# Kernel tuning notes

Measured on AMD Instinct MI355X. Metric: run time of the kernel, lower is better.

## Reference

```python
import jax, jax.numpy as jnp
import numpy as np

COMMITMENT_WEIGHT = 1.0


def setup_inputs() -> dict:
    key = jax.random.key(0)
    k1, k2 = jax.random.split(key)
    clap_embeddings = jax.random.normal(k1, (16, 2048, 512), dtype=jnp.float32)
    # Learned codebooks for the 8 residual quantizer stages: [Q, C, D]
    codebooks = jax.random.normal(k2, (8, 1024, 512), dtype=jnp.float32)
    return {"clap_embeddings": clap_embeddings, "codebooks": codebooks}


def reference(clap_embeddings, codebooks):
    """Residual VQ: cascade of nearest-codebook lookups on the residual.
    Returns (quantized [B,T,D], indices [B,T,Q], commit_loss scalar)."""
    B, T, D = clap_embeddings.shape
    flat = clap_embeddings.reshape(-1, D)  # [N, D], N = B*T

    def step(carry, cb):
        residual, quant_acc = carry          # [N,D], [N,D]; cb: [C,D]
        cb_sq = jnp.sum(cb * cb, axis=-1)    # [C]
        # squared-dist argmin: ||r||^2 term is constant per row, drop it
        dists = cb_sq[None, :] - 2.0 * (residual @ cb.T)  # [N, C]
        idx = jnp.argmin(dists, axis=-1)     # [N]
        qv = cb[idx]                         # [N, D] gather
        # commitment loss: mse(detach(quantize), residual_input)
        loss = jnp.mean(jnp.square(jax.lax.stop_gradient(qv) - residual))
        # straight-through estimator
        qv_st = residual + jax.lax.stop_gradient(qv - residual)
        new_residual = residual - jax.lax.stop_gradient(qv)
        return (new_residual, quant_acc + qv_st), (idx, loss)

    init = (flat, jnp.zeros_like(flat))
    (_, quant_flat), (idx_q, losses) = jax.lax.scan(step, init, codebooks)

    quantized = quant_flat.reshape(B, T, D)
    indices = jnp.transpose(idx_q, (1, 0)).reshape(B, T, -1)  # [B, T, Q]
    commit_loss = jnp.sum(losses) * COMMITMENT_WEIGHT
    return quantized, indices, commit_loss
```

## Files before the change

### kernel.cpp

```cpp
#include <hip/hip_runtime.h>
#include <hip/hip_bf16.h>

#define NQ 8
#define NC 1024
#define ND 512
#define NROWTOT 32768
#define QOFF 16777216ULL
#define TAU2 0.05f
#define RST 260

typedef short short8 __attribute__((ext_vector_type(8)));
typedef float f32x16 __attribute__((ext_vector_type(16)));

__device__ __forceinline__ unsigned f2bf_u(float f) {
  unsigned u = __float_as_uint(f);
  return (u + 0x7FFFu + ((u >> 16) & 1u)) >> 16;
}
__device__ __forceinline__ void merge_in(float &d1, int &i1, float &d2, int &i2,
                                         float nd, int ni) {
  bool b1 = (nd < d1) || (nd == d1 && ni < i1);
  bool b2 = (nd < d2) || (nd == d2 && ni < i2);
  if (b1) { d2 = d1; i2 = i1; d1 = nd; i1 = ni; }
  else if (b2) { d2 = nd; i2 = ni; }
}

__global__ __launch_bounds__(256) void cbsq_kernel(const float* __restrict__ cbg,
                                                   float* __restrict__ ws) {
  const int tid = threadIdx.x, wv = tid >> 6, lane = tid & 63;
  const int cbase = blockIdx.x * 32 + wv * 8;
  for (int j = 0; j < 8; ++j) {
    const int c = cbase + j;
    const float4* p = reinterpret_cast<const float4*>(cbg + (size_t)c * ND + lane * 8);
    float4 a = p[0], b = p[1];
    float s = a.x*a.x + a.y*a.y + a.z*a.z + a.w*a.w
            + b.x*b.x + b.y*b.y + b.z*b.z + b.w*b.w;
    #pragma unroll
    for (int m = 1; m < 64; m <<= 1) s += __shfl_xor(s, m, 64);
    if (lane == 0) ws[c] = s;
  }
}

__global__ __launch_bounds__(256) void fmt_kernel(const float* __restrict__ cbg,
                                                  unsigned short* __restrict__ Bh,
                                                  unsigned short* __restrict__ Bl) {
  int t = blockIdx.x * 256 + threadIdx.x;
  int i16 = t & 1023, ks = (t >> 10) & 31, cp = (t >> 15) & 1, q = (t >> 16) & 7;
  int grp = i16 >> 9, col = i16 & 511, c = cp * 512 + col;
  const float* src = cbg + ((size_t)q * NC + c) * ND + ks * 16 + grp * 8;
  float4 a = reinterpret_cast<const float4*>(src)[0];
  float4 b = reinterpret_cast<const float4*>(src)[1];
  float v[8] = {a.x, a.y, a.z, a.w, b.x, b.y, b.z, b.w};
  unsigned short hv[8], lv[8];
  #pragma unroll
  for (int j = 0; j < 8; ++j) {
    unsigned hb = f2bf_u(v[j]);
    float hf = __uint_as_float(hb << 16);
    unsigned lb = f2bf_u(v[j] - hf);
    hv[j] = (unsigned short)hb; lv[j] = (unsigned short)lb;
  }
  size_t dst = (size_t)(t >> 10) * 8192 + (size_t)i16 * 8;
  uint4 wh, wl;
  wh.x = hv[0] | ((unsigned)hv[1] << 16); wh.y = hv[2] | ((unsigned)hv[3] << 16);
  wh.z = hv[4] | ((unsigned)hv[5] << 16); wh.w = hv[6] | ((unsigned)hv[7] << 16);
  wl.x = lv[0] | ((unsigned)lv[1] << 16); wl.y = lv[2] | ((unsigned)lv[3] << 16);
  wl.z = lv[4] | ((unsigned)lv[5] << 16); wl.w = lv[6] | ((unsigned)lv[7] << 16);
  *reinterpret_cast<uint4*>(Bh + dst) = wh;
  *reinterpret_cast<uint4*>(Bl + dst) = wl;
}

__global__ __launch_bounds__(256) void copy_kernel(const float4* __restrict__ src,
                                                   float4* __restrict__ dst) {
  int i = blockIdx.x * 256 + threadIdx.x;
  dst[i] = src[i];
}

__global__ __launch_bounds__(1024) __attribute__((amdgpu_waves_per_eu(4, 4)))
void dist_kernel(const float* __restrict__ resf, const float* __restrict__ cbsq_g,
                 const unsigned short* __restrict__ Bh,
                 const unsigned short* __restrict__ Bl,
                 float* __restrict__ t2d, int* __restrict__ t2i, int q) {
  __shared__ unsigned resH[64 * RST];
  __shared__ unsigned resL[64 * RST];
  __shared__ float mrgd[2][8][64][2];
  __shared__ int   mrgi[2][8][64][2];
  const int tid = threadIdx.x;
  const int w = tid >> 6, l = tid & 63;
  const int n0 = blockIdx.x * 64;
  const int rowbase = (w >> 3) * 32;
  const int colq = (w & 7) * 64;
  union U8 { uint4 q4; short8 s; unsigned u[4]; };

  {
    const float4* src = reinterpret_cast<const float4*>(resf) + (size_t)n0 * 128;
    #pragma unroll
    for (int j = 0; j < 8; ++j) {
      const int idx = j * 1024 + tid;
      float4 v = src[idx];
      const int row = idx >> 7, c4 = idx & 127;
      unsigned h0 = f2bf_u(v.x), g0 = f2bf_u(v.x - __uint_as_float(h0 << 16));
      unsigned h1 = f2bf_u(v.y), g1 = f2bf_u(v.y - __uint_as_float(h1 << 16));
      unsigned h2 = f2bf_u(v.z), g2 = f2bf_u(v.z - __uint_as_float(h2 << 16));
      unsigned h3 = f2bf_u(v.w), g3 = f2bf_u(v.w - __uint_as_float(h3 << 16));
      const int off = row * RST + c4 * 2;
      resH[off]     = h0 | (h1 << 16);
      resH[off + 1] = h2 | (h3 << 16);
      resL[off]     = g0 | (g1 << 16);
      resL[off + 1] = g2 | (g3 << 16);
    }
  }

  int baddr[2];
  #pragma unroll
  for (int t = 0; t < 2; ++t) {
    int i16 = ((l >> 5) << 9) + colq + t * 32 + (l & 31);
    baddr[t] = i16 * 8;
  }
  const int aoff0 = (rowbase + (l & 31)) * RST + ((l >> 5) << 2);
  __syncthreads();

  #pragma unroll 1
  for (int cp = 0; cp < 2; ++cp) {
    f32x16 acc[2];
    #pragma unroll
    for (int t = 0; t < 2; ++t)
      #pragma unroll
      for (int e = 0; e < 16; ++e) acc[t][e] = 0.f;

    const unsigned short* bhc = Bh + (size_t)((q * 2 + cp) * 32) * 8192;
    const unsigned short* blc = Bl + (size_t)((q * 2 + cp) * 32) * 8192;
    float sqv[2];
    #pragma unroll
    for (int t = 0; t < 2; ++t)
      sqv[t] = cbsq_g[q * NC + cp * 512 + colq + t * 32 + (l & 31)];

    uint4 fA[4], fB[4];

#define LOADB(buf, kk) { \
    const unsigned short* _h = bhc + (size_t)(kk) * 8192; \
    const unsigned short* _l = blc + (size_t)(kk) * 8192; \
    buf[0] = *reinterpret_cast<const uint4*>(_h + baddr[0]); \
    buf[1] = *reinterpret_cast<const uint4*>(_h + baddr[1]); \
    buf[2] = *reinterpret_cast<const uint4*>(_l + baddr[0]); \
    buf[3] = *reinterpret_cast<const uint4*>(_l + baddr[1]); }

#define DOSTEP(kk, buf) { \
    U8 Ah, Al; \
    const int _a = aoff0 + (kk) * 8; \
    Ah.q4 = *reinterpret_cast<const uint4*>(&resH[_a]); \
    Al.q4 = *reinterpret_cast<const uint4*>(&resL[_a]); \
    U8 b0h, b1h, b0l, b1l; \
    b0h.q4 = buf[0]; b1h.q4 = buf[1]; b0l.q4 = buf[2]; b1l.q4 = buf[3]; \
    acc[0] = __builtin_amdgcn_mfma_f32_32x32x16_bf16(Ah.s, b0h.s, acc[0], 0, 0, 0); \
    acc[0] = __builtin_amdgcn_mfma_f32_32x32x16_bf16(Al.s, b0h.s, acc[0], 0, 0, 0); \
    acc[0] = __builtin_amdgcn_mfma_f32_32x32x16_bf16(Ah.s, b0l.s, acc[0], 0, 0, 0); \
    acc[1] = __builtin_amdgcn_mfma_f32_32x32x16_bf16(Ah.s, b1h.s, acc[1], 0, 0, 0); \
    acc[1] = __builtin_amdgcn_mfma_f32_32x32x16_bf16(Al.s, b1h.s, acc[1], 0, 0, 0); \
    acc[1] = __builtin_amdgcn_mfma_f32_32x32x16_bf16(Ah.s, b1l.s, acc[1], 0, 0, 0); }

    LOADB(fA, 0);
    #pragma unroll 1
    for (int ks = 0; ks < 32; ks += 2) {
      LOADB(fB, ks + 1);
      DOSTEP(ks, fA);
      LOADB(fA, ks + 2 < 32 ? ks + 2 : 0);
      DOSTEP(ks + 1, fB);
    }
#undef LOADB
#undef DOSTEP

    #pragma unroll
    for (int rg2 = 0; rg2 < 16; ++rg2) {
      float d1 = INFINITY, d2 = INFINITY; int i1 = 0x7fffffff, i2 = 0x7fffffff;
      #pragma unroll
      for (int t = 0; t < 2; ++t) {
        int col = cp * 512 + colq + t * 32 + (l & 31);
        float dd = sqv[t] - 2.0f * acc[t][rg2];
        merge_in(d1, i1, d2, i2, dd, col);
      }
      #pragma unroll
      for (int m = 1; m < 32; m <<= 1) {
        float od1 = __shfl_xor(d1, m, 64), od2 = __shfl_xor(d2, m, 64);
        int oi1 = __shfl_xor(i1, m, 64), oi2 = __shfl_xor(i2, m, 64);
        merge_in(d1, i1, d2, i2, od1, oi1);
        merge_in(d1, i1, d2, i2, od2, oi2);
      }
      if ((l & 31) == 0) {
        int h = l >> 5;
        int rr = rowbase + (rg2 & 3) + 8 * (rg2 >> 2) + 4 * h;
        mrgd[cp][w & 7][rr][0] = d1; mrgd[cp][w & 7][rr][1] = d2;
        mrgi[cp][w & 7][rr][0] = i1; mrgi[cp][w & 7][rr][1] = i2;
      }
    }
  }
  __syncthreads();

  if (tid < 64) {
    float d1 = INFINITY, d2 = INFINITY; int i1 = 0x7fffffff, i2 = 0x7fffffff;
    #pragma unroll
    for (int c2 = 0; c2 < 2; ++c2)
      #pragma unroll
      for (int s2 = 0; s2 < 8; ++s2) {
        merge_in(d1, i1, d2, i2, mrgd[c2][s2][tid][0], mrgi[c2][s2][tid][0]);
        merge_in(d1, i1, d2, i2, mrgd[c2][s2][tid][1], mrgi[c2][s2][tid][1]);
      }
    t2d[(size_t)(n0 + tid) * 2 + 0] = d1;
    t2d[(size_t)(n0 + tid) * 2 + 1] = d2;
    t2i[(size_t)(n0 + tid) * 2 + 0] = i1;
    t2i[(size_t)(n0 + tid) * 2 + 1] = i2;
  }
}

__global__ __launch_bounds__(256) void upd_kernel(
    float* __restrict__ outf, const float* __restrict__ emb,
    const float* __restrict__ cbg, const float* __restrict__ t2d,
    const int* __restrict__ t2i, float* __restrict__ lpart, int q) {
  __shared__ int   fi_sh[64];
  __shared__ int   tlist[64][3];
  __shared__ int   tcount;
  __shared__ float red[256];
  const int tid = threadIdx.x;
  const int w = tid >> 6, l = tid & 63;
  const int n0 = blockIdx.x * 64;

  if (tid == 0) tcount = 0;
  __syncthreads();

  if (tid < 64) {
    float d1 = t2d[(size_t)(n0 + tid) * 2 + 0];
    float d2 = t2d[(size_t)(n0 + tid) * 2 + 1];
    int i1 = t2i[(size_t)(n0 + tid) * 2 + 0];
    int i2 = t2i[(size_t)(n0 + tid) * 2 + 1];
    int fi = i1 < 0 ? 0 : (i1 > NC - 1 ? NC - 1 : i1);
    int ib = i2 < 0 ? 0 : (i2 > NC - 1 ? NC - 1 : i2);
    fi_sh[tid] = fi;
    if (d2 - d1 < TAU2 && ib != fi) {
      int p = atomicAdd(&tcount, 1);
      tlist[p][0] = tid; tlist[p][1] = fi; tlist[p][2] = ib;
    }
  }
  __syncthreads();

  {
    int nt_ = tcount;
    for (int it = w; it < nt_; it += 4) {
      int rr = tlist[it][0], ia = tlist[it][1], ib = tlist[it][2];
      const float4* rp = reinterpret_cast<const float4*>(outf + (size_t)(n0 + rr) * ND + l * 8);
      float4 r0 = rp[0], r1 = rp[1];
      float rv[8] = {r0.x, r0.y, r0.z, r0.w, r1.x, r1.y, r1.z, r1.w};
      double da = 0.0, db = 0.0;
      {
        const float4* cr = reinterpret_cast<const float4*>(
            cbg + ((size_t)q * NC + ia) * ND + l * 8);
        float4 c0 = cr[0], c1 = cr[1];
        float cv[8] = {c0.x,c0.y,c0.z,c0.w,c1.x,c1.y,c1.z,c1.w};
        #pragma unroll
        for (int j = 0; j < 8; ++j) { double e = (double)cv[j] - (double)rv[j]; da += e * e; }
      }
      {
        const float4* cr = reinterpret_cast<const float4*>(
            cbg + ((size_t)q * NC + ib) * ND + l * 8);
        float4 c0 = cr[0], c1 = cr[1];
        float cv[8] = {c0.x,c0.y,c0.z,c0.w,c1.x,c1.y,c1.z,c1.w};
        #pragma unroll
        for (int j = 0; j < 8; ++j) { double e = (double)cv[j] - (double)rv[j]; db += e * e; }
      }
      #pragma unroll
      for (int m = 1; m < 64; m <<= 1) { da += __shfl_xor(da, m, 64); db += __shfl_xor(db, m, 64); }
      if (l == 0 && (db < da || (db == da && ib < ia))) fi_sh[rr] = ib;
    }
  }
  __syncthreads();

  if (tid < 64)
    outf[QOFF + (size_t)(n0 + tid) * NQ + q] = (float)fi_sh[tid];

  {
    const int row = tid >> 2, sg = tid & 3;
    const size_t base = (size_t)(n0 + row) * ND + sg * 128;
    float4* op = reinterpret_cast<float4*>(outf + base);
    const float4* cp4 = reinterpret_cast<const float4*>(
        cbg + ((size_t)q * NC + fi_sh[row]) * ND + sg * 128);
    const float4* ep = reinterpret_cast<const float4*>(emb + base);
    float ls = 0.f;
    #pragma unroll 4
    for (int i = 0; i < 32; ++i) {
      float4 r = op[i], c = cp4[i];
      float4 nr;
      nr.x = r.x - c.x; nr.y = r.y - c.y; nr.z = r.z - c.z; nr.w = r.w - c.w;
      ls += nr.x*nr.x + nr.y*nr.y + nr.z*nr.z + nr.w*nr.w;
      if (q < NQ - 1) {
        op[i] = nr;
      } else {
        float4 e = ep[i];
        float4 qv;
        qv.x = e.x - nr.x; qv.y = e.y - nr.y; qv.z = e.z - nr.z; qv.w = e.w - nr.w;
        op[i] = qv;
      }
    }
    red[tid] = ls;
  }
  __syncthreads();
  for (int s = 128; s > 0; s >>= 1) {
    if (tid < s) red[tid] += red[tid + s];
    __syncthreads();
  }
  if (tid == 0) lpart[blockIdx.x * NQ + q] = red[0];
}

__global__ __launch_bounds__(256) void loss_kernel(const float* __restrict__ lossws,
                                                   int n, float* __restrict__ outf) {
  __shared__ float red[256];
  const int tid = threadIdx.x;
  float s = 0.f;
  for (int i = tid; i < n; i += 256) s += lossws[i];
  red[tid] = s;
  __syncthreads();
  for (int w = 128; w > 0; w >>= 1) {
    if (tid < w) red[tid] += red[tid + w];
    __syncthreads();
  }
  if (tid == 0) outf[QOFF + (size_t)NROWTOT * NQ] = red[0] / 16777216.0f;
}

#define ROWS 32
#define BK 32
#define CP 512
#define TAU 0.05f

__global__ __launch_bounds__(256, 1) void rvq_fb(
    const float* __restrict__ emb, const float* __restrict__ cbg,
    const float* __restrict__ cbsq, float* __restrict__ lossws,
    float* __restrict__ outf) {
  __shared__ float resT[ND][ROWS];
  __shared__ float cc[BK][CP];
  __shared__ int   idx_sh[ROWS];
  __shared__ float wred[4];

  const int tid = threadIdx.x;
  const int wv = tid >> 6, lane = tid & 63;
  const int rg = wv, cg = lane;
  const int n0 = blockIdx.x * ROWS;

  float qacc[64];
  #pragma unroll
  for (int s = 0; s < 64; ++s) qacc[s] = 0.f;

  {
    const int r = tid & 31, db = tid >> 5;
    const float4* src = reinterpret_cast<const float4*>(emb + (size_t)(n0 + r) * ND + db * 64);
    #pragma unroll
    for (int s = 0; s < 16; ++s) {
      float4 v = src[s];
      int d = db * 64 + s * 4;
      resT[d+0][r] = v.x; resT[d+1][r] = v.y; resT[d+2][r] = v.z; resT[d+3][r] = v.w;
    }
  }
  __syncthreads();

  const int c0l = cg * 8;
  const int swm = (c0l >> 6) << 2;
  const int off0 = c0l ^ swm;
  const int off1 = (c0l + 4) ^ swm;

  for (int q = 0; q < NQ; ++q) {
    const float* cbq = cbg + (size_t)q * NC * ND;
    float bd1[8], bd2[8]; int bi1[8], bi2[8];
    #pragma unroll
    for (int j = 0; j < 8; ++j) { bd1[j]=INFINITY; bd2[j]=INFINITY; bi1[j]=0x7fffffff; bi2[j]=0x7fffffff; }

    for (int cp = 0; cp < 2; ++cp) {
      float acc[8][8];
      #pragma unroll
      for (int a = 0; a < 8; ++a)
        #pragma unroll
        for (int b = 0; b < 8; ++b) acc[a][b] = 0.f;

      for (int kc = 0; kc < ND / BK; ++kc) {
        __syncthreads();
        {
          const int half = tid & 1;
          const int k0 = half * 16;
          #pragma unroll
          for (int it = 0; it < 4; ++it) {
            const int c = (tid >> 1) + it * 128;
            const int pc = c ^ ((c >> 6) << 2);
            const float4* src = reinterpret_cast<const float4*>(
                cbq + (size_t)(cp * CP + c) * ND + kc * BK + half * 16);
            float4 v0 = src[0], v1 = src[1], v2 = src[2], v3 = src[3];
            cc[k0+ 0][pc]=v0.x; cc[k0+ 1][pc]=v0.y; cc[k0+ 2][pc]=v0.z; cc[k0+ 3][pc]=v0.w;
            cc[k0+ 4][pc]=v1.x; cc[k0+ 5][pc]=v1.y; cc[k0+ 6][pc]=v1.z; cc[k0+ 7][pc]=v1.w;
            cc[k0+ 8][pc]=v2.x; cc[k0+ 9][pc]=v2.y; cc[k0+10][pc]=v2.z; cc[k0+11][pc]=v2.w;
            cc[k0+12][pc]=v3.x; cc[k0+13][pc]=v3.y; cc[k0+14][pc]=v3.z; cc[k0+15][pc]=v3.w;
          }
        }
        __syncthreads();

        float tmp[8][8];
        #pragma unroll
        for (int a = 0; a < 8; ++a)
          #pragma unroll
          for (int b = 0; b < 8; ++b) tmp[a][b] = 0.f;

        #pragma unroll
        for (int kk = 0; kk < BK; ++kk) {
          const float4* rp = reinterpret_cast<const float4*>(&resT[kc * BK + kk][rg * 8]);
          float4 r0 = rp[0], r1 = rp[1];
          const float* ccrow = &cc[kk][0];
          float4 c0 = *reinterpret_cast<const float4*>(ccrow + off0);
          float4 c1 = *reinterpret_cast<const float4*>(ccrow + off1);
          float rv[8] = {r0.x, r0.y, r0.z, r0.w, r1.x, r1.y, r1.z, r1.w};
          float cv[8] = {c0.x, c0.y, c0.z, c0.w, c1.x, c1.y, c1.z, c1.w};
          #pragma unroll
          for (int a = 0; a < 8; ++a)
            #pragma unroll
            for (int b = 0; b < 8; ++b)
              tmp[a][b] = fmaf(rv[a], cv[b], tmp[a][b]);
        }
        #pragma unroll
        for (int a = 0; a < 8; ++a)
          #pragma unroll
          for (int b = 0; b < 8; ++b) acc[a][b] += tmp[a][b];
      }

      const float4* qp = reinterpret_cast<const float4*>(cbsq + q * NC + cp * CP + cg * 8);
      float4 s0 = qp[0], s1 = qp[1];
      float sqv[8] = {s0.x, s0.y, s0.z, s0.w, s1.x, s1.y, s1.z, s1.w};
      #pragma unroll
      for (int r = 0; r < 8; ++r) {
        float d1 = INFINITY, d2 = INFINITY; int i1 = 0x7fffffff, i2 = 0x7fffffff;
        #pragma unroll
        for (int j = 0; j < 8; ++j) {
          float dd = sqv[j] - 2.0f * acc[r][j];
          merge_in(d1, i1, d2, i2, dd, cp * CP + cg * 8 + j);
        }
        #pragma unroll
        for (int m = 1; m < 64; m <<= 1) {
          float od1 = __shfl_xor(d1, m, 64), od2 = __shfl_xor(d2, m, 64);
          int oi1 = __shfl_xor(i1, m, 64), oi2 = __shfl_xor(i2, m, 64);
          merge_in(d1, i1, d2, i2, od1, oi1);
          merge_in(d1, i1, d2, i2, od2, oi2);
        }
        merge_in(bd1[r], bi1[r], bd2[r], bi2[r], d1, i1);
        merge_in(bd1[r], bi1[r], bd2[r], bi2[r], d2, i2);
      }
    }

    #pragma unroll 1
    for (int r = 0; r < 8; ++r) {
      int fi = bi1[r];
      if (bd2[r] - bd1[r] < TAU) {
        const int row = rg * 8 + r;
        const int ia = bi1[r], ib = bi2[r];
        double da = 0.0, db2 = 0.0;
        #pragma unroll 1
        for (int t = 0; t < 2; ++t) {
          const int cidx = t ? ib : ia;
          const float* cr = cbq + (size_t)cidx * ND;
          double dot = 0.0, ss = 0.0;
          #pragma unroll
          for (int u = 0; u < 8; ++u) {
            int k = lane * 8 + u;
            double cvv = (double)cr[k];
            double rvv = (double)resT[k][row];
            dot += cvv * rvv; ss += cvv * cvv;
          }
          #pragma unroll
          for (int m = 1; m < 64; m <<= 1) { dot += __shfl_xor(dot, m, 64); ss += __shfl_xor(ss, m, 64); }
          double dd = ss - 2.0 * dot;
          if (t) db2 = dd; else da = dd;
        }
        if (db2 < da || (db2 == da && ib < ia)) fi = ib;
      }
      fi = fi < 0 ? 0 : (fi > NC - 1 ? NC - 1 : fi);
      if (lane == 0) {
        idx_sh[rg * 8 + r] = fi;
        outf[QOFF + (size_t)(n0 + rg * 8 + r) * NQ + q] = (float)fi;
      }
    }
    __syncthreads();

    {
      const int r = tid & 31, db = tid >> 5;
      const float* crow = cbq + (size_t)idx_sh[r] * ND;
      float ls = 0.f;
      #pragma unroll
      for (int s = 0; s < 64; ++s) {
        int d = db * 64 + s;
        float cv = crow[d];
        float nv = resT[d][r] - cv;
        resT[d][r] = nv;
        qacc[s] += cv;
        ls += nv * nv;
      }
      #pragma unroll
      for (int m = 1; m < 64; m <<= 1) ls += __shfl_xor(ls, m, 64);
      if (lane == 0) wred[wv] = ls;
    }
    __syncthreads();
    if (tid == 0) lossws[blockIdx.x * NQ + q] = wred[0] + wred[1] + wred[2] + wred[3];
    __syncthreads();
  }

  {
    const int r = tid & 31, db = tid >> 5;
    #pragma unroll
    for (int g = 0; g < 16; ++g) {
      float4 w2;
      w2.x = qacc[g*4+0]; w2.y = qacc[g*4+1]; w2.z = qacc[g*4+2]; w2.w = qacc[g*4+3];
      *reinterpret_cast<float4*>(outf + (size_t)(n0 + r) * ND + db * 64 + g * 4) = w2;
    }
  }
}

extern "C" void kernel_launch(void* const* d_in, const int* in_sizes, int n_in,
                              void* d_out, int out_size, void* d_ws, size_t ws_size,
                              hipStream_t stream) {
  (void)in_sizes; (void)n_in; (void)out_size;
  const float* emb = (const float*)d_in[0];
  const float* cbg = (const float*)d_in[1];
  float* wsf = (float*)d_ws;
  float* outf = (float*)d_out;

  cbsq_kernel<<<256, 256, 0, stream>>>(cbg, wsf);

  if (ws_size >= (size_t)18 * 1024 * 1024) {
    float* lpart = wsf + 8192;
    unsigned short* Bh = (unsigned short*)((char*)d_ws + 65536);
    unsigned short* Bl = Bh + 4194304;
    float* t2d = (float*)((char*)d_ws + 16842752);
    int*   t2i = (int*)((char*)d_ws + 17104896);

    fmt_kernel<<<2048, 256, 0, stream>>>(cbg, Bh, Bl);
    copy_kernel<<<16384, 256, 0, stream>>>((const float4*)emb, (float4*)outf);
    for (int q = 0; q < NQ; ++q) {
      dist_kernel<<<512, 1024, 0, stream>>>(outf, wsf, Bh, Bl, t2d, t2i, q);
      upd_kernel<<<512, 256, 0, stream>>>(outf, emb, cbg, t2d, t2i, lpart, q);
    }
    loss_kernel<<<1, 256, 0, stream>>>(lpart, 4096, outf);
  } else {
    rvq_fb<<<1024, 256, 0, stream>>>(emb, cbg, wsf, wsf + 8192, outf);
    loss_kernel<<<1, 256, 0, stream>>>(wsf + 8192, 8192, outf);
  }
}
```

Measured before the change: 4.596 ms.

## Shrink dist tile to 32 rows, pack hi/lo bf16 in LDS, add sched barriers

The distance kernel now uses 512-thread blocks covering 32 rows each, launched as 1024 blocks with launch bounds (512,2) so two blocks can share a CU. The residual's hi and lo bf16 halves are packed together into one LDS word per element and split back into the MFMA operands with shifts and masks at use time. Scheduling barriers pin the order of the prefetch and MFMA steps. Each block now reloads the full codebook tile for only half as many rows, which doubles codebook traffic per row and adds ALU work for unpacking, in exchange for better occupancy and a smaller LDS footprint per block.

Result: no change. 4.542 ms (-1.2%).

```diff
diff --git a/kernel.cpp b/kernel.cpp
--- a/kernel.cpp
+++ b/kernel.cpp
@@ -7,7 +7,7 @@
 #define NROWTOT 32768
 #define QOFF 16777216ULL
 #define TAU2 0.05f
-#define RST 260
+#define RSTP 522
 
 typedef short short8 __attribute__((ext_vector_type(8)));
 typedef float f32x16 __attribute__((ext_vector_type(16)));
@@ -15,6 +15,12 @@
 __device__ __forceinline__ unsigned f2bf_u(float f) {
   unsigned u = __float_as_uint(f);
   return (u + 0x7FFFu + ((u >> 16) & 1u)) >> 16;
+}
+__device__ __forceinline__ unsigned pack_hl(float x) {
+  unsigned hb = f2bf_u(x);
+  float hf = __uint_as_float(hb << 16);
+  unsigned lb = f2bf_u(x - hf);
+  return (hb << 16) | lb;
 }
 __device__ __forceinline__ void merge_in(float &d1, int &i1, float &d2, int &i2,
                                          float nd, int ni) {
@@ -74,38 +80,32 @@
   dst[i] = src[i];
 }
 
-__global__ __launch_bounds__(1024) __attribute__((amdgpu_waves_per_eu(4, 4)))
+__global__ __launch_bounds__(512, 2)
 void dist_kernel(const float* __restrict__ resf, const float* __restrict__ cbsq_g,
                  const unsigned short* __restrict__ Bh,
                  const unsigned short* __restrict__ Bl,
                  float* __restrict__ t2d, int* __restrict__ t2i, int q) {
-  __shared__ unsigned resH[64 * RST];
-  __shared__ unsigned resL[64 * RST];
-  __shared__ float mrgd[2][8][64][2];
-  __shared__ int   mrgi[2][8][64][2];
+  __shared__ unsigned resP[32 * RSTP];
+  __shared__ float mrgd[2][8][32][2];
+  __shared__ int   mrgi[2][8][32][2];
   const int tid = threadIdx.x;
   const int w = tid >> 6, l = tid & 63;
-  const int n0 = blockIdx.x * 64;
-  const int rowbase = (w >> 3) * 32;
-  const int colq = (w & 7) * 64;
+  const int n0 = blockIdx.x * 32;
+  const int colq = w * 64;
   union U8 { uint4 q4; short8 s; unsigned u[4]; };
 
   {
     const float4* src = reinterpret_cast<const float4*>(resf) + (size_t)n0 * 128;
     #pragma unroll
     for (int j = 0; j < 8; ++j) {
-      const int idx = j * 1024 + tid;
+      const int idx = j * 512 + tid;
       float4 v = src[idx];
       const int row = idx >> 7, c4 = idx & 127;
-      unsigned h0 = f2bf_u(v.x), g0 = f2bf_u(v.x - __uint_as_float(h0 << 16));
-      unsigned h1 = f2bf_u(v.y), g1 = f2bf_u(v.y - __uint_as_float(h1 << 16));
-      unsigned h2 = f2bf_u(v.z), g2 = f2bf_u(v.z - __uint_as_float(h2 << 16));
-      unsigned h3 = f2bf_u(v.w), g3 = f2bf_u(v.w - __uint_as_float(h3 << 16));
-      const int off = row * RST + c4 * 2;
-      resH[off]     = h0 | (h1 << 16);
-      resH[off + 1] = h2 | (h3 << 16);
-      resL[off]     = g0 | (g1 << 16);
-      resL[off + 1] = g2 | (g3 << 16);
+      const int off = row * RSTP + c4 * 4;
+      resP[off + 0] = pack_hl(v.x);
+      resP[off + 1] = pack_hl(v.y);
+      resP[off + 2] = pack_hl(v.z);
+      resP[off + 3] = pack_hl(v.w);
     }
   }
 
@@ -115,7 +115,7 @@
     int i16 = ((l >> 5) << 9) + colq + t * 32 + (l & 31);
     baddr[t] = i16 * 8;
   }
-  const int aoff0 = (rowbase + (l & 31)) * RST + ((l >> 5) << 2);
+  const int aoff0 = (l & 31) * RSTP + ((l >> 5) << 3);
   __syncthreads();
 
   #pragma unroll 1
@@ -135,19 +135,26 @@
 
     uint4 fA[4], fB[4];
 
+#define SB() __builtin_amdgcn_sched_barrier(0)
+
 #define LOADB(buf, kk) { \
-    const unsigned short* _h = bhc + (size_t)(kk) * 8192; \
-    const unsigned short* _l = blc + (size_t)(kk) * 8192; \
+    const unsigned short* _h = bhc + (size_t)((kk) & 31) * 8192; \
+    const unsigned short* _l = blc + (size_t)((kk) & 31) * 8192; \
     buf[0] = *reinterpret_cast<const uint4*>(_h + baddr[0]); \
     buf[1] = *reinterpret_cast<const uint4*>(_h + baddr[1]); \
     buf[2] = *reinterpret_cast<const uint4*>(_l + baddr[0]); \
     buf[3] = *reinterpret_cast<const uint4*>(_l + baddr[1]); }
 
 #define DOSTEP(kk, buf) { \
+    uint4 p0 = *reinterpret_cast<const uint4*>(&resP[aoff0 + (kk) * 16]); \
+    uint4 p1 = *reinterpret_cast<const uint4*>(&resP[aoff0 + (kk) * 16 + 4]); \
+    unsigned pp[8] = {p0.x, p0.y, p0.z, p0.w, p1.x, p1.y, p1.z, p1.w}; \
     U8 Ah, Al; \
-    const int _a = aoff0 + (kk) * 8; \
-    Ah.q4 = *reinterpret_cast<const uint4*>(&resH[_a]); \
-    Al.q4 = *reinterpret_cast<const uint4*>(&resL[_a]); \
+    _Pragma("unroll") \
+    for (int p2 = 0; p2 < 4; ++p2) { \
+      Ah.u[p2] = (pp[2*p2] >> 16) | (pp[2*p2+1] & 0xFFFF0000u); \
+      Al.u[p2] = (pp[2*p2] & 0xFFFFu) | (pp[2*p2+1] << 16); \
+    } \
     U8 b0h, b1h, b0l, b1l; \
     b0h.q4 = buf[0]; b1h.q4 = buf[1]; b0l.q4 = buf[2]; b1l.q4 = buf[3]; \
     acc[0] = __builtin_amdgcn_mfma_f32_32x32x16_bf16(Ah.s, b0h.s, acc[0], 0, 0, 0); \
@@ -158,15 +165,17 @@
     acc[1] = __builtin_amdgcn_mfma_f32_32x32x16_bf16(Ah.s, b1l.s, acc[1], 0, 0, 0); }
 
     LOADB(fA, 0);
+    SB();
     #pragma unroll 1
     for (int ks = 0; ks < 32; ks += 2) {
-      LOADB(fB, ks + 1);
-      DOSTEP(ks, fA);
-      LOADB(fA, ks + 2 < 32 ? ks + 2 : 0);
-      DOSTEP(ks + 1, fB);
+      LOADB(fB, ks + 1); SB();
+      DOSTEP(ks + 0, fA); SB();
+      LOADB(fA, ks + 2); SB();
+      DOSTEP(ks + 1, fB); SB();
     }
 #undef LOADB
 #undef DOSTEP
+#undef SB
 
     #pragma unroll
     for (int rg2 = 0; rg2 < 16; ++rg2) {
@@ -186,15 +195,15 @@
       }
       if ((l & 31) == 0) {
         int h = l >> 5;
-        int rr = rowbase + (rg2 & 3) + 8 * (rg2 >> 2) + 4 * h;
-        mrgd[cp][w & 7][rr][0] = d1; mrgd[cp][w & 7][rr][1] = d2;
-        mrgi[cp][w & 7][rr][0] = i1; mrgi[cp][w & 7][rr][1] = i2;
-      }
-    }
-  }
-  __syncthreads();
-
-  if (tid < 64) {
+        int rr = (rg2 & 3) + 8 * (rg2 >> 2) + 4 * h;
+        mrgd[cp][w][rr][0] = d1; mrgd[cp][w][rr][1] = d2;
+        mrgi[cp][w][rr][0] = i1; mrgi[cp][w][rr][1] = i2;
+      }
+    }
+  }
+  __syncthreads();
+
+  if (tid < 32) {
     float d1 = INFINITY, d2 = INFINITY; int i1 = 0x7fffffff, i2 = 0x7fffffff;
     #pragma unroll
     for (int c2 = 0; c2 < 2; ++c2)
@@ -533,7 +542,7 @@
     fmt_kernel<<<2048, 256, 0, stream>>>(cbg, Bh, Bl);
     copy_kernel<<<16384, 256, 0, stream>>>((const float4*)emb, (float4*)outf);
     for (int q = 0; q < NQ; ++q) {
-      dist_kernel<<<512, 1024, 0, stream>>>(outf, wsf, Bh, Bl, t2d, t2i, q);
+      dist_kernel<<<1024, 512, 0, stream>>>(outf, wsf, Bh, Bl, t2d, t2i, q);
       upd_kernel<<<512, 256, 0, stream>>>(outf, emb, cbg, t2d, t2i, lpart, q);
     }
     loss_kernel<<<1, 256, 0, stream>>>(lpart, 4096, outf);
```
